# Performance work log

Measured on AMD Instinct MI355X. Metric: run time of the kernel, lower is better.

The kernel has to match this reference:

```python
import jax, jax.numpy as jnp
import numpy as np
from jax import lax

DIM, GC1, GC2, GC3 = 128, 32, 64, 32
B, H, W = 4, 128, 128
EPS = 1e-5


def conv2d(x, w, b, pad, dilation=1, groups=1):
    y = lax.conv_general_dilated(x, w, (1, 1), [(pad, pad), (pad, pad)],
                                 rhs_dilation=(dilation, dilation),
                                 feature_group_count=groups,
                                 dimension_numbers=('NCHW', 'OIHW', 'NCHW'))
    return y + b[None, :, None, None]


def bilinear_gather(img, ys, xs):
    # img [B,C,H,W]; ys,xs [B,K,H,W] float sample coords. Zero padding outside.
    b, c, h, w = img.shape
    k = ys.shape[1]
    flat = img.reshape(b, c, h * w)
    y0 = jnp.floor(ys)
    x0 = jnp.floor(xs)
    acc = jnp.zeros((b, c, k, h, w), img.dtype)
    for dy in (0, 1):
        for dx in (0, 1):
            yc = y0 + dy
            xc = x0 + dx
            wgt = (1.0 - jnp.abs(ys - yc)) * (1.0 - jnp.abs(xs - xc))
            valid = (yc >= 0) & (yc <= h - 1) & (xc >= 0) & (xc <= w - 1)
            yi = jnp.clip(yc, 0, h - 1).astype(jnp.int32)
            xi = jnp.clip(xc, 0, w - 1).astype(jnp.int32)
            idx = (yi * w + xi).reshape(b, 1, k * h * w)
            g = jnp.take_along_axis(flat, jnp.broadcast_to(idx, (b, c, k * h * w)), axis=2)
            g = g.reshape(b, c, k, h, w)
            acc = acc + g * (wgt * valid.astype(img.dtype))[:, None]
    return acc


def deform_depthwise(x, off, w):
    # x [B,C,H,W], off [B,2*9,H,W] (dy,dx interleaved per kernel tap), w [C,9]
    b, c, h, ww = x.shape
    off = off.reshape(b, 9, 2, h, ww)
    dy, dx = off[:, :, 0], off[:, :, 1]  # [B,9,H,W]
    ks = jnp.arange(3, dtype=x.dtype)
    kyy = jnp.repeat(ks, 3)  # [9]
    kxx = jnp.tile(ks, 3)
    iy = jnp.arange(h, dtype=x.dtype)
    jx = jnp.arange(ww, dtype=x.dtype)
    ys = iy[None, None, :, None] - 1.0 + kyy[None, :, None, None] + dy
    xs = jx[None, None, None, :] - 1.0 + kxx[None, :, None, None] + dx
    sampled = bilinear_gather(x, ys, xs)  # [B,C,9,H,W]
    return jnp.einsum('bckhw,ck->bchw', sampled, w)


def batchnorm(x, g, b):
    mu = jnp.mean(x, axis=(0, 2, 3), keepdims=True)
    var = jnp.var(x, axis=(0, 2, 3), keepdims=True)
    return (x - mu) * lax.rsqrt(var + EPS) * g[None, :, None, None] + b[None, :, None, None]


def setup_inputs() -> dict:
    key = jax.random.key(0)
    ks = jax.random.split(key, 16)
    s = 0.05
    return {
        'x': jax.random.normal(ks[0], (B, DIM, H, W), jnp.float32),
        'offset_w': jax.random.normal(ks[1], (18, GC1, 3, 3), jnp.float32) * s,
        'offset_b': jax.random.normal(ks[2], (18,), jnp.float32) * s,
        'deform_w': jax.random.normal(ks[3], (GC1, 9), jnp.float32) * s,
        'dw_w': jax.random.normal(ks[4], (GC2, 1, 7, 7), jnp.float32) * s,
        'dw_b': jax.random.normal(ks[5], (GC2,), jnp.float32) * s,
        'dw2_w': jax.random.normal(ks[6], (GC3, GC3, 3, 3), jnp.float32) * s,
        'dw2_b': jax.random.normal(ks[7], (GC3,), jnp.float32) * s,
        'bn1_g': jnp.ones((DIM,), jnp.float32),
        'bn1_b': jnp.zeros((DIM,), jnp.float32),
        'w1': jax.random.normal(ks[8], (DIM, 4 * DIM), jnp.float32) * s,
        'b1': jax.random.normal(ks[9], (4 * DIM,), jnp.float32) * s,
        'w2': jax.random.normal(ks[10], (4 * DIM, DIM), jnp.float32) * s,
        'b2': jax.random.normal(ks[11], (DIM,), jnp.float32) * s,
        'bn2_g': jnp.ones((DIM,), jnp.float32),
        'bn2_b': jnp.zeros((DIM,), jnp.float32),
    }


def reference(x, offset_w, offset_b, deform_w, dw_w, dw_b, dw2_w, dw2_b,
              bn1_g, bn1_b, w1, b1, w2, b2, bn2_g, bn2_b):
    x_hw, x_w, x_h = jnp.split(x, [GC1, GC1 + GC2], axis=1)
    off = conv2d(x_hw, offset_w, offset_b, pad=1)
    d0 = deform_depthwise(x_hw, off, deform_w)
    d1 = conv2d(x_w, dw_w, dw_b, pad=3, groups=GC2)          # 7x7 depthwise
    d2 = conv2d(x_h, dw2_w, dw2_b, pad=2, dilation=2)        # 3x3 dense, dilation 2
    y = jnp.concatenate([d0, d1, d2], axis=1)
    # channel shuffle, groups=2
    b, c, h, w = y.shape
    y = y.reshape(b, 2, c // 2, h, w).transpose(0, 2, 1, 3, 4).reshape(b, c, h, w)
    y = batchnorm(y, bn1_g, bn1_b)
    t = y.transpose(0, 2, 3, 1)                               # [B,H,W,C]
    t = jax.nn.gelu(t @ w1 + b1, approximate=False)
    t = t @ w2 + b2
    y = t.transpose(0, 3, 1, 2)
    y = batchnorm(y, bn2_g, bn2_b)
    return jax.nn.gelu(x + y, approximate=False)
```

## Files before the change

kernel.cpp:

```cpp
#include <hip/hip_runtime.h>
#include <hip/hip_bf16.h>
#include <math.h>

#define BB 4
#define CC 128
#define HH 128
#define WWD 128
#define HWW 16384
#define PREC 17424

typedef __attribute__((ext_vector_type(8))) short bf16x8;
typedef __attribute__((ext_vector_type(4))) float floatx4;
typedef __attribute__((ext_vector_type(4))) unsigned short us4;
typedef __attribute__((ext_vector_type(8))) unsigned short us8;

__device__ __forceinline__ float gelu_exact(float v) {
  return 0.5f * v * (1.0f + erff(v * 0.70710678118654752f));
}
__device__ __forceinline__ unsigned short f2us(float f) {
  union { float f; unsigned int u; } c; c.f = f;
  unsigned int u = c.u;
  return (unsigned short)((u + 0x7FFFu + ((u >> 16) & 1u)) >> 16);
}

__global__ __launch_bounds__(256) void k_zero(unsigned short* __restrict__ xp) {
  long i = ((long)blockIdx.x * 256 + threadIdx.x) * 8;
  us8 z = (us8)0;
  *(us8*)&xp[i] = z;
}

__global__ __launch_bounds__(256) void k_xt(
    const float* __restrict__ x, float* __restrict__ xt) {
  __shared__ float t[64 * 33];
  int bid = blockIdx.x;
  int tid = threadIdx.x;
  int b = bid >> 8, pg = bid & 255;
  int c = tid >> 3, g8 = tid & 7;
  const float* xp = x + ((long)b * CC + c) * HWW + pg * 64 + g8 * 8;
  float4 v0 = *(const float4*)xp;
  float4 v1 = *(const float4*)(xp + 4);
  t[(g8 * 8 + 0) * 33 + c] = v0.x; t[(g8 * 8 + 1) * 33 + c] = v0.y;
  t[(g8 * 8 + 2) * 33 + c] = v0.z; t[(g8 * 8 + 3) * 33 + c] = v0.w;
  t[(g8 * 8 + 4) * 33 + c] = v1.x; t[(g8 * 8 + 5) * 33 + c] = v1.y;
  t[(g8 * 8 + 6) * 33 + c] = v1.z; t[(g8 * 8 + 7) * 33 + c] = v1.w;
  __syncthreads();
  int u = tid >> 2, q = tid & 3;
  float4 o0, o1;
  o0.x = t[u * 33 + q * 8 + 0]; o0.y = t[u * 33 + q * 8 + 1];
  o0.z = t[u * 33 + q * 8 + 2]; o0.w = t[u * 33 + q * 8 + 3];
  o1.x = t[u * 33 + q * 8 + 4]; o1.y = t[u * 33 + q * 8 + 5];
  o1.z = t[u * 33 + q * 8 + 6]; o1.w = t[u * 33 + q * 8 + 7];
  float* d = xt + ((long)b * HWW + pg * 64 + u) * 32 + q * 8;
  *(float4*)d = o0;
  *(float4*)(d + 4) = o1;
}

__global__ __launch_bounds__(256) void k_pack(
    const float* __restrict__ x, unsigned short* __restrict__ xp) {
  __shared__ float t[64 * 33];
  int bid = blockIdx.x;
  int tid = threadIdx.x;
  int which = bid >> 10, b = (bid >> 8) & 3, pg = bid & 255;
  int cbase = which ? 96 : 0;
  int c = tid >> 3, g8 = tid & 7;
  const float* xpr = x + ((long)b * CC + cbase + c) * HWW + pg * 64 + g8 * 8;
  float4 v0 = *(const float4*)xpr;
  float4 v1 = *(const float4*)(xpr + 4);
  t[(g8 * 8 + 0) * 33 + c] = v0.x; t[(g8 * 8 + 1) * 33 + c] = v0.y;
  t[(g8 * 8 + 2) * 33 + c] = v0.z; t[(g8 * 8 + 3) * 33 + c] = v0.w;
  t[(g8 * 8 + 4) * 33 + c] = v1.x; t[(g8 * 8 + 5) * 33 + c] = v1.y;
  t[(g8 * 8 + 6) * 33 + c] = v1.z; t[(g8 * 8 + 7) * 33 + c] = v1.w;
  __syncthreads();
  int u = tid >> 2, q = tid & 3;
  int p = pg * 64 + u;
  int yy = p >> 7, xx = p & 127;
  long rec = (long)(which * 4 + b) * PREC + (yy + 2) * 132 + xx + 2;
  us8 o;
#pragma unroll
  for (int k = 0; k < 8; k++) o[k] = f2us(t[u * 33 + q * 8 + k]);
  *(us8*)&xp[rec * 32 + q * 8] = o;
}

__global__ __launch_bounds__(256) void k_wprep2(
    const float* __restrict__ offw, const float* __restrict__ dilw,
    unsigned short* __restrict__ wob, unsigned short* __restrict__ w3b) {
  int t = blockIdx.x * 256 + threadIdx.x;
  if (t >= 2304) return;
  int which = t >= 1152;
  int u = t - which * 1152;
  int lane = u & 63, tn = u >> 6;
  int col = lane & 15, quad = lane >> 4;
  int tap = tn >> 1, nt = tn & 1;
  int n = nt * 16 + col;
  const float* W = which ? dilw : offw;
  int noc = which ? 32 : 18;
  unsigned short* d = (which ? w3b : wob) + (long)(tn * 64 + lane) * 8;
#pragma unroll
  for (int j = 0; j < 8; j++)
    d[j] = (n < noc) ? f2us(W[(long)n * 288 + (quad * 8 + j) * 9 + tap]) : (unsigned short)0;
}

__global__ __launch_bounds__(256) void k_offc_mm(
    const unsigned short* __restrict__ xp0, const unsigned short* __restrict__ wob,
    const float* __restrict__ bias, float* __restrict__ off) {
  int bid = blockIdx.x;
  int b = bid >> 7, yy = bid & 127;
  int tid = threadIdx.x;
  int lane = tid & 63, wv = tid >> 6;
  int row = lane & 15, quad = lane >> 4;
  const unsigned short* plane = xp0 + (long)b * PREC * 32;
  int xb = wv * 32;
  floatx4 Oa[2][2];
#pragma unroll
  for (int mt = 0; mt < 2; mt++)
#pragma unroll
    for (int nt = 0; nt < 2; nt++) Oa[mt][nt] = (floatx4)0.f;
#pragma unroll
  for (int t = 0; t < 9; t++) {
    int dy = t / 3 - 1, dx = t % 3 - 1;
    const unsigned short* rp = plane + ((long)(yy + 2 + dy) * 132 + 2 + dx + xb) * 32;
    bf16x8 A0 = *(const bf16x8*)&rp[row * 32 + quad * 8];
    bf16x8 A1 = *(const bf16x8*)&rp[(16 + row) * 32 + quad * 8];
#pragma unroll
    for (int nt = 0; nt < 2; nt++) {
      bf16x8 Bf = *(const bf16x8*)&wob[(long)((t * 2 + nt) * 64 + lane) * 8];
      Oa[0][nt] = __builtin_amdgcn_mfma_f32_16x16x32_bf16(A0, Bf, Oa[0][nt], 0, 0, 0);
      Oa[1][nt] = __builtin_amdgcn_mfma_f32_16x16x32_bf16(A1, Bf, Oa[1][nt], 0, 0, 0);
    }
  }
#pragma unroll
  for (int nt = 0; nt < 2; nt++) {
    int oc = nt * 16 + (lane & 15);
    if (oc < 18) {
      float bb = bias[oc];
#pragma unroll
      for (int mt = 0; mt < 2; mt++) {
        floatx4 v = Oa[mt][nt];
        v[0] += bb; v[1] += bb; v[2] += bb; v[3] += bb;
        long p = (long)(b * 18 + oc) * HWW + yy * 128 + xb + mt * 16 + quad * 4;
        *(floatx4*)&off[p] = v;
      }
    }
  }
}

__global__ __launch_bounds__(256) void k_dil3_mm(
    const unsigned short* __restrict__ xp1, const unsigned short* __restrict__ w3b,
    const float* __restrict__ bias, float* __restrict__ y) {
  int bid = blockIdx.x;
  int b = bid >> 7, yy = bid & 127;
  int tid = threadIdx.x;
  int lane = tid & 63, wv = tid >> 6;
  int row = lane & 15, quad = lane >> 4;
  const unsigned short* plane = xp1 + (long)b * PREC * 32;
  int xb = wv * 32;
  floatx4 Oa[2][2];
#pragma unroll
  for (int mt = 0; mt < 2; mt++)
#pragma unroll
    for (int nt = 0; nt < 2; nt++) Oa[mt][nt] = (floatx4)0.f;
#pragma unroll
  for (int t = 0; t < 9; t++) {
    int dy = (t / 3 - 1) * 2, dx = (t % 3 - 1) * 2;
    const unsigned short* rp = plane + ((long)(yy + 2 + dy) * 132 + 2 + dx + xb) * 32;
    bf16x8 A0 = *(const bf16x8*)&rp[row * 32 + quad * 8];
    bf16x8 A1 = *(const bf16x8*)&rp[(16 + row) * 32 + quad * 8];
#pragma unroll
    for (int nt = 0; nt < 2; nt++) {
      bf16x8 Bf = *(const bf16x8*)&w3b[(long)((t * 2 + nt) * 64 + lane) * 8];
      Oa[0][nt] = __builtin_amdgcn_mfma_f32_16x16x32_bf16(A0, Bf, Oa[0][nt], 0, 0, 0);
      Oa[1][nt] = __builtin_amdgcn_mfma_f32_16x16x32_bf16(A1, Bf, Oa[1][nt], 0, 0, 0);
    }
  }
#pragma unroll
  for (int nt = 0; nt < 2; nt++) {
    int oc = nt * 16 + (lane & 15);
    int cp = 65 + 2 * oc;
    float bb = bias[oc];
#pragma unroll
    for (int mt = 0; mt < 2; mt++) {
      floatx4 v = Oa[mt][nt];
      v[0] += bb; v[1] += bb; v[2] += bb; v[3] += bb;
      long p = ((long)b * CC + cp) * HWW + yy * 128 + xb + mt * 16 + quad * 4;
      *(floatx4*)&y[p] = v;
    }
  }
}

__global__ __launch_bounds__(256) void k_deform(
    const float* __restrict__ xt, const float* __restrict__ off,
    const float* __restrict__ dw, float* __restrict__ y) {
  __shared__ float wl[144];
  int tid = threadIdx.x;
  int g = blockIdx.x * 256 + tid;
  int hf = g >> 16;
  int pix = g & 65535;
  if (tid < 144) {
    int k = tid >> 4, q = tid & 15;
    wl[k * 16 + q] = dw[(hf * 16 + q) * 9 + k];
  }
  __syncthreads();
  int b = pix >> 14, p = pix & 16383;
  int i = p >> 7, j = p & 127;
  float acc[16];
#pragma unroll
  for (int q = 0; q < 16; q++) acc[q] = 0.f;
  const float* offb = off + (long)b * 18 * HWW + p;
  const float* xb = xt + (long)b * HWW * 32 + hf * 16;
  for (int k = 0; k < 9; k++) {
    float dy = offb[(long)(2 * k) * HWW];
    float dx = offb[(long)(2 * k + 1) * HWW];
    float ys = (float)i - 1.f + (float)(k / 3) + dy;
    float xs = (float)j - 1.f + (float)(k % 3) + dx;
    float y0 = floorf(ys), x0 = floorf(xs);
    float fy = ys - y0, fx = xs - x0;
    int iy0 = (int)y0, ix0 = (int)x0;
    int iy1 = iy0 + 1, ix1 = ix0 + 1;
    float wy0 = (1.f - fy) * ((iy0 >= 0 && iy0 <= 127) ? 1.f : 0.f);
    float wy1 = fy * ((iy1 >= 0 && iy1 <= 127) ? 1.f : 0.f);
    float wx0 = (1.f - fx) * ((ix0 >= 0 && ix0 <= 127) ? 1.f : 0.f);
    float wx1 = fx * ((ix1 >= 0 && ix1 <= 127) ? 1.f : 0.f);
    int cy0 = min(max(iy0, 0), 127), cy1 = min(max(iy1, 0), 127);
    int cx0 = min(max(ix0, 0), 127), cx1 = min(max(ix1, 0), 127);
    int ci[4] = {cy0 * 128 + cx0, cy0 * 128 + cx1, cy1 * 128 + cx0, cy1 * 128 + cx1};
    float cw[4] = {wy0 * wx0, wy0 * wx1, wy1 * wx0, wy1 * wx1};
    float v[16];
#pragma unroll
    for (int q = 0; q < 16; q++) v[q] = 0.f;
#pragma unroll
    for (int cn = 0; cn < 4; cn++) {
      const float* cp = xb + (long)ci[cn] * 32;
      float wc = cw[cn];
      float4 p0 = *(const float4*)cp;
      float4 p1 = *(const float4*)(cp + 4);
      float4 p2 = *(const float4*)(cp + 8);
      float4 p3 = *(const float4*)(cp + 12);
      v[0] += wc * p0.x;  v[1] += wc * p0.y;  v[2] += wc * p0.z;  v[3] += wc * p0.w;
      v[4] += wc * p1.x;  v[5] += wc * p1.y;  v[6] += wc * p1.z;  v[7] += wc * p1.w;
      v[8] += wc * p2.x;  v[9] += wc * p2.y;  v[10] += wc * p2.z; v[11] += wc * p2.w;
      v[12] += wc * p3.x; v[13] += wc * p3.y; v[14] += wc * p3.z; v[15] += wc * p3.w;
    }
    const float* wr = &wl[k * 16];
#pragma unroll
    for (int q = 0; q < 16; q++) acc[q] += wr[q] * v[q];
  }
#pragma unroll
  for (int q = 0; q < 16; q++) {
    int cp = 2 * (hf * 16 + q);
    y[((long)b * CC + cp) * HWW + p] = acc[q];
  }
}

__global__ __launch_bounds__(256) void k_dw7(
    const float* __restrict__ x, const float* __restrict__ w,
    const float* __restrict__ bias, float* __restrict__ y) {
  __shared__ float tile[22 * 136];
  __shared__ float wl[49];
  __shared__ float bsh;
  int bid = blockIdx.x;
  int b = bid >> 9, m = (bid >> 3) & 63, strip = bid & 7;
  int r0 = strip * 16;
  int tid = threadIdx.x;
  const float* xp = x + ((long)b * CC + 32 + m) * HWW;
  for (int idx = tid; idx < 2948; idx += 256) {
    int rr = idx / 134;
    int cc = idx - rr * 134 - 3;
    int gy = r0 - 3 + rr;
    float v = 0.f;
    if ((unsigned)gy < 128u && (unsigned)cc < 128u) v = xp[gy * 128 + cc];
    tile[rr * 136 + cc + 3] = v;
  }
  if (tid < 49) wl[tid] = w[m * 49 + tid];
  if (tid == 64) bsh = bias[m];
  __syncthreads();
  int j = tid & 127, s = tid >> 7;
  float acc[8];
#pragma unroll
  for (int o = 0; o < 8; o++) acc[o] = bsh;
#pragma unroll
  for (int kx = 0; kx < 7; kx++) {
#pragma unroll
    for (int rr = 0; rr < 14; rr++) {
      float v = tile[(s * 8 + rr) * 136 + j + kx];
      int olo = rr - 6 > 0 ? rr - 6 : 0;
      int ohi = rr < 7 ? rr : 7;
#pragma unroll
      for (int o = 0; o < 8; o++) {
        if (o >= olo && o <= ohi) acc[o] += v * wl[(rr - o) * 7 + kx];
      }
    }
  }
  int c = 32 + m;
  int cp = (c & 63) * 2 + (c >> 6);
  float* yp = y + ((long)b * CC + cp) * HWW;
#pragma unroll
  for (int o = 0; o < 8; o++) {
    yp[(r0 + s * 8 + o) * 128 + j] = acc[o];
  }
}

__global__ __launch_bounds__(256) void k_stats1(
    const float* __restrict__ buf, float* __restrict__ part) {
  __shared__ float sh[256], sh2[256];
  int c = blockIdx.x >> 2, b = blockIdx.x & 3;
  int tid = threadIdx.x;
  const float* p = buf + ((long)b * CC + c) * HWW;
  float s = 0.f, s2 = 0.f;
  for (int it = 0; it < 16; it++) {
    float4 v = *(const float4*)(p + (it * 256 + tid) * 4);
    s += v.x + v.y + v.z + v.w;
    s2 += v.x * v.x + v.y * v.y + v.z * v.z + v.w * v.w;
  }
  sh[tid] = s; sh2[tid] = s2;
  __syncthreads();
  for (int o = 128; o > 0; o >>= 1) {
    if (tid < o) { sh[tid] += sh[tid + o]; sh2[tid] += sh2[tid + o]; }
    __syncthreads();
  }
  if (tid == 0) {
    part[blockIdx.x * 2] = sh[0];
    part[blockIdx.x * 2 + 1] = sh2[0];
  }
}

__global__ __launch_bounds__(128) void k_stats2(
    const float* __restrict__ part, float* __restrict__ mean, float* __restrict__ istd) {
  int c = threadIdx.x;
  float s = 0.f, s2 = 0.f;
#pragma unroll
  for (int b = 0; b < 4; b++) {
    s += part[(c * 4 + b) * 2];
    s2 += part[(c * 4 + b) * 2 + 1];
  }
  float mu = s * (1.f / 65536.f);
  float var = s2 * (1.f / 65536.f) - mu * mu;
  mean[c] = mu;
  istd[c] = rsqrtf(var + 1e-5f);
}

__global__ __launch_bounds__(256) void k_wprep(
    const float* __restrict__ w1, const float* __restrict__ w2,
    unsigned short* __restrict__ w1b, unsigned short* __restrict__ w2b) {
  int t = blockIdx.x * 256 + threadIdx.x;
  int which = t >> 13;
  int u = t & 8191;
  int lane = u & 63;
  int ntks = u >> 6;
  int col = lane & 15, quad = lane >> 4;
  if (which == 0) {
    int nt = ntks >> 2, ks = ntks & 3;
    int n = nt * 16 + col;
    int k0 = ks * 32 + quad * 8;
    unsigned short* d = w1b + (long)u * 8;
#pragma unroll
    for (int j = 0; j < 8; j++) d[j] = f2us(w1[(long)(k0 + j) * 512 + n]);
  } else {
    int nt = ntks >> 4, ks = ntks & 15;
    int n = nt * 16 + col;
    int k0 = ks * 32 + quad * 8;
    unsigned short* d = w2b + (long)u * 8;
#pragma unroll
    for (int j = 0; j < 8; j++) d[j] = f2us(w2[(long)(k0 + j) * 128 + n]);
  }
}

__global__ __launch_bounds__(256, 2) void k_mlp_mfma(
    const float* __restrict__ y, const float* __restrict__ mean1,
    const float* __restrict__ istd1, const float* __restrict__ g1,
    const float* __restrict__ b1n, const unsigned short* __restrict__ w1b,
    const float* __restrict__ b1, const unsigned short* __restrict__ w2b,
    const float* __restrict__ b2, float* __restrict__ tmid) {
  __shared__ unsigned short At[128 * 136];
  __shared__ unsigned short Hs[4 * 32 * 72];
  __shared__ float scs[128], shs[128];
  int tid = threadIdx.x;
  int lane = tid & 63, wv = tid >> 6;
  int row = lane & 15, quad = lane >> 4;
  int n0 = blockIdx.x * 128;
  int b = n0 >> 14;
  long base = (long)b * CC * HWW + (n0 & 16383);
  if (tid < 128) {
    float sc = istd1[tid] * g1[tid];
    scs[tid] = sc;
    shs[tid] = b1n[tid] - mean1[tid] * sc;
  }
  __syncthreads();
  for (int it = 0; it < 16; it++) {
    int u = it * 256 + tid;
    int tok = u & 127, cg = u >> 7;
    us4 wvv;
#pragma unroll
    for (int r = 0; r < 4; r++) {
      int c = cg * 4 + r;
      float v = y[base + (long)c * HWW + tok];
      wvv[r] = f2us(v * scs[c] + shs[c]);
    }
    *(us4*)&At[tok * 136 + cg * 4] = wvv;
  }
  __syncthreads();
  bf16x8 Af[2][4];
#pragma unroll
  for (int mt = 0; mt < 2; mt++)
#pragma unroll
    for (int ks = 0; ks < 4; ks++)
      Af[mt][ks] = *(const bf16x8*)&At[(wv * 32 + mt * 16 + row) * 136 + ks * 32 + quad * 8];

  floatx4 Oa[2][8];
#pragma unroll
  for (int mt = 0; mt < 2; mt++)
#pragma unroll
    for (int nt = 0; nt < 8; nt++) Oa[mt][nt] = (floatx4)0.f;

  const int wvb = wv * 32 * 72;
  for (int ch = 0; ch < 8; ch++) {
    floatx4 Ha[2][4];
#pragma unroll
    for (int mt = 0; mt < 2; mt++)
#pragma unroll
      for (int nt = 0; nt < 4; nt++) Ha[mt][nt] = (floatx4)0.f;
#pragma unroll
    for (int nt = 0; nt < 4; nt++) {
      int ntg = ch * 4 + nt;
#pragma unroll
      for (int ks = 0; ks < 4; ks++) {
        bf16x8 Bf = *(const bf16x8*)&w1b[(long)(((ntg * 4 + ks) << 6) + lane) * 8];
        Ha[0][nt] = __builtin_amdgcn_mfma_f32_16x16x32_bf16(Af[0][ks], Bf, Ha[0][nt], 0, 0, 0);
        Ha[1][nt] = __builtin_amdgcn_mfma_f32_16x16x32_bf16(Af[1][ks], Bf, Ha[1][nt], 0, 0, 0);
      }
    }
#pragma unroll
    for (int nt = 0; nt < 4; nt++) {
      float bb = b1[ch * 64 + nt * 16 + row];
#pragma unroll
      for (int mt = 0; mt < 2; mt++)
#pragma unroll
        for (int r = 0; r < 4; r++) {
          float h = gelu_exact(Ha[mt][nt][r] + bb);
          Hs[wvb + (mt * 16 + quad * 4 + r) * 72 + nt * 16 + row] = f2us(h);
        }
    }
    __syncthreads();
    bf16x8 A2[2][2];
#pragma unroll
    for (int mt = 0; mt < 2; mt++)
#pragma unroll
      for (int ks = 0; ks < 2; ks++)
        A2[mt][ks] = *(const bf16x8*)&Hs[wvb + (mt * 16 + row) * 72 + ks * 32 + quad * 8];
#pragma unroll
    for (int nt = 0; nt < 8; nt++) {
#pragma unroll
      for (int ks = 0; ks < 2; ks++) {
        bf16x8 Bf = *(const bf16x8*)&w2b[(long)(((nt * 16 + ch * 2 + ks) << 6) + lane) * 8];
        Oa[0][nt] = __builtin_amdgcn_mfma_f32_16x16x32_bf16(A2[0][ks], Bf, Oa[0][nt], 0, 0, 0);
        Oa[1][nt] = __builtin_amdgcn_mfma_f32_16x16x32_bf16(A2[1][ks], Bf, Oa[1][nt], 0, 0, 0);
      }
    }
    __syncthreads();
  }
#pragma unroll
  for (int nt = 0; nt < 8; nt++) {
    int c = nt * 16 + row;
    float bb = b2[c];
    long op = base + (long)c * HWW + wv * 32 + quad * 4;
#pragma unroll
    for (int mt = 0; mt < 2; mt++) {
      floatx4 vv = Oa[mt][nt];
      vv[0] += bb; vv[1] += bb; vv[2] += bb; vv[3] += bb;
      *(floatx4*)&tmid[op + mt * 16] = vv;
    }
  }
}

__global__ __launch_bounds__(256) void k_final(
    const float* __restrict__ x, const float* __restrict__ mean2,
    const float* __restrict__ istd2, const float* __restrict__ g2,
    const float* __restrict__ b2n, float* __restrict__ out) {
  long e4 = (long)blockIdx.x * 256 + threadIdx.x;
  int c = (int)((e4 >> 12) & 127);
  float sc = istd2[c] * g2[c];
  float sh = b2n[c] - mean2[c] * sc;
  float4 o = *(float4*)&out[e4 * 4];
  float4 xv = *(const float4*)&x[e4 * 4];
  o.x = gelu_exact(xv.x + o.x * sc + sh);
  o.y = gelu_exact(xv.y + o.y * sc + sh);
  o.z = gelu_exact(xv.z + o.z * sc + sh);
  o.w = gelu_exact(xv.w + o.w * sc + sh);
  *(float4*)&out[e4 * 4] = o;
}

extern "C" void kernel_launch(void* const* d_in, const int* in_sizes, int n_in,
                              void* d_out, int out_size, void* d_ws, size_t ws_size,
                              hipStream_t stream) {
  const float* x        = (const float*)d_in[0];
  const float* offset_w = (const float*)d_in[1];
  const float* offset_b = (const float*)d_in[2];
  const float* deform_w = (const float*)d_in[3];
  const float* dw_w     = (const float*)d_in[4];
  const float* dw_b     = (const float*)d_in[5];
  const float* dw2_w    = (const float*)d_in[6];
  const float* dw2_b    = (const float*)d_in[7];
  const float* bn1_g    = (const float*)d_in[8];
  const float* bn1_b    = (const float*)d_in[9];
  const float* w1       = (const float*)d_in[10];
  const float* b1       = (const float*)d_in[11];
  const float* w2       = (const float*)d_in[12];
  const float* b2       = (const float*)d_in[13];
  const float* bn2_g    = (const float*)d_in[14];
  const float* bn2_b    = (const float*)d_in[15];
  float* out = (float*)d_out;

  float* ws    = (float*)d_ws;
  float* off   = ws;
  float* ybuf  = ws + 1179648;
  float* stats = ws + 9568256;
  float* mean1 = stats, *istd1 = stats + 128;
  float* mean2 = stats + 256, *istd2 = stats + 384;
  unsigned short* w1b = (unsigned short*)(ws + 9568768);
  unsigned short* w2b = (unsigned short*)(ws + 9601536);
  float* part  = ws + 9634304;
  float* xt    = ws + 9635328;
  unsigned short* wob = (unsigned short*)(ws + 11732480);
  unsigned short* w3b = (unsigned short*)(ws + 11737088);
  unsigned short* xp  = (unsigned short*)(ws + 11741696);
  unsigned short* xp0 = xp;
  unsigned short* xp1 = xp + (long)4 * PREC * 32;
  float* tmid  = out;

  k_zero<<<2178, 256, 0, stream>>>(xp);
  k_wprep<<<64, 256, 0, stream>>>(w1, w2, w1b, w2b);
  k_wprep2<<<9, 256, 0, stream>>>(offset_w, dw2_w, wob, w3b);
  k_pack<<<2048, 256, 0, stream>>>(x, xp);
  k_xt<<<1024, 256, 0, stream>>>(x, xt);
  k_offc_mm<<<512, 256, 0, stream>>>(xp0, wob, offset_b, off);
  k_deform<<<512, 256, 0, stream>>>(xt, off, deform_w, ybuf);
  k_dw7<<<2048, 256, 0, stream>>>(x, dw_w, dw_b, ybuf);
  k_dil3_mm<<<512, 256, 0, stream>>>(xp1, w3b, dw2_b, ybuf);
  k_stats1<<<512, 256, 0, stream>>>(ybuf, part);
  k_stats2<<<1, 128, 0, stream>>>(part, mean1, istd1);
  k_mlp_mfma<<<512, 256, 0, stream>>>(ybuf, mean1, istd1, bn1_g, bn1_b, w1b, b1, w2b, b2, tmid);
  k_stats1<<<512, 256, 0, stream>>>(tmid, part);
  k_stats2<<<1, 128, 0, stream>>>(part, mean2, istd2);
  k_final<<<8192, 256, 0, stream>>>(x, mean2, istd2, bn2_g, bn2_b, out);
}
```

Measured before the change: 278.7 us.

## Fuse BN2 statistics into MLP epilogue and drop inner-loop barriers

The MLP kernel now accumulates per-channel sum and sum-of-squares of its output in shared memory, then adds them atomically to a global buffer. This removes the separate stats pass that re-read the full MLP output, and a zeroing block is added to the existing zero kernel. The first GEMM swaps its operands so each lane holds four consecutive hidden units, which allows vectorized bias loads and us4 stores into the per-wave hidden buffer. Both __syncthreads in the chunk loop are removed because each wave only touches its own Hs slice. The global float atomics make the BN2 statistics order-nondeterministic.

Result: no change. 280.8 us (+0.7%).

```diff
diff --git a/kernel.cpp b/kernel.cpp
--- a/kernel.cpp
+++ b/kernel.cpp
@@ -23,7 +23,9 @@
   return (unsigned short)((u + 0x7FFFu + ((u >> 16) & 1u)) >> 16);
 }
 
-__global__ __launch_bounds__(256) void k_zero(unsigned short* __restrict__ xp) {
+__global__ __launch_bounds__(256) void k_zero(
+    unsigned short* __restrict__ xp, float* __restrict__ part2) {
+  if (blockIdx.x == 2178) { part2[threadIdx.x] = 0.f; return; }
   long i = ((long)blockIdx.x * 256 + threadIdx.x) * 8;
   us8 z = (us8)0;
   *(us8*)&xp[i] = z;
@@ -338,6 +340,15 @@
   istd[c] = rsqrtf(var + 1e-5f);
 }
 
+__global__ __launch_bounds__(128) void k_stats2b(
+    const float* __restrict__ part2, float* __restrict__ mean, float* __restrict__ istd) {
+  int c = threadIdx.x;
+  float mu = part2[c] * (1.f / 65536.f);
+  float var = part2[128 + c] * (1.f / 65536.f) - mu * mu;
+  mean[c] = mu;
+  istd[c] = rsqrtf(var + 1e-5f);
+}
+
 __global__ __launch_bounds__(256) void k_wprep(
     const float* __restrict__ w1, const float* __restrict__ w2,
     unsigned short* __restrict__ w1b, unsigned short* __restrict__ w2b) {
@@ -369,10 +380,12 @@
     const float* __restrict__ istd1, const float* __restrict__ g1,
     const float* __restrict__ b1n, const unsigned short* __restrict__ w1b,
     const float* __restrict__ b1, const unsigned short* __restrict__ w2b,
-    const float* __restrict__ b2, float* __restrict__ tmid) {
+    const float* __restrict__ b2, float* __restrict__ tmid,
+    float* __restrict__ part2) {
   __shared__ unsigned short At[128 * 136];
   __shared__ unsigned short Hs[4 * 32 * 72];
   __shared__ float scs[128], shs[128];
+  __shared__ float ps[128], ps2[128];
   int tid = threadIdx.x;
   int lane = tid & 63, wv = tid >> 6;
   int row = lane & 15, quad = lane >> 4;
@@ -383,6 +396,7 @@
     float sc = istd1[tid] * g1[tid];
     scs[tid] = sc;
     shs[tid] = b1n[tid] - mean1[tid] * sc;
+    ps[tid] = 0.f; ps2[tid] = 0.f;
   }
   __syncthreads();
   for (int it = 0; it < 16; it++) {
@@ -413,33 +427,34 @@
 
   const int wvb = wv * 32 * 72;
   for (int ch = 0; ch < 8; ch++) {
-    floatx4 Ha[2][4];
-#pragma unroll
-    for (int mt = 0; mt < 2; mt++)
-#pragma unroll
-      for (int nt = 0; nt < 4; nt++) Ha[mt][nt] = (floatx4)0.f;
+    floatx4 Ha[4][2];
+#pragma unroll
+    for (int nt = 0; nt < 4; nt++)
+#pragma unroll
+      for (int mt = 0; mt < 2; mt++) Ha[nt][mt] = (floatx4)0.f;
 #pragma unroll
     for (int nt = 0; nt < 4; nt++) {
-      int ntg = ch * 4 + nt;
+      int ht = ch * 4 + nt;
 #pragma unroll
       for (int ks = 0; ks < 4; ks++) {
-        bf16x8 Bf = *(const bf16x8*)&w1b[(long)(((ntg * 4 + ks) << 6) + lane) * 8];
-        Ha[0][nt] = __builtin_amdgcn_mfma_f32_16x16x32_bf16(Af[0][ks], Bf, Ha[0][nt], 0, 0, 0);
-        Ha[1][nt] = __builtin_amdgcn_mfma_f32_16x16x32_bf16(Af[1][ks], Bf, Ha[1][nt], 0, 0, 0);
+        bf16x8 Wf = *(const bf16x8*)&w1b[(long)(((ht * 4 + ks) << 6) + lane) * 8];
+        Ha[nt][0] = __builtin_amdgcn_mfma_f32_16x16x32_bf16(Wf, Af[0][ks], Ha[nt][0], 0, 0, 0);
+        Ha[nt][1] = __builtin_amdgcn_mfma_f32_16x16x32_bf16(Wf, Af[1][ks], Ha[nt][1], 0, 0, 0);
       }
     }
 #pragma unroll
     for (int nt = 0; nt < 4; nt++) {
-      float bb = b1[ch * 64 + nt * 16 + row];
-#pragma unroll
-      for (int mt = 0; mt < 2; mt++)
-#pragma unroll
-        for (int r = 0; r < 4; r++) {
-          float h = gelu_exact(Ha[mt][nt][r] + bb);
-          Hs[wvb + (mt * 16 + quad * 4 + r) * 72 + nt * 16 + row] = f2us(h);
-        }
-    }
-    __syncthreads();
+      float4 bb = *(const float4*)&b1[ch * 64 + nt * 16 + quad * 4];
+#pragma unroll
+      for (int mt = 0; mt < 2; mt++) {
+        us4 hv;
+        hv[0] = f2us(gelu_exact(Ha[nt][mt][0] + bb.x));
+        hv[1] = f2us(gelu_exact(Ha[nt][mt][1] + bb.y));
+        hv[2] = f2us(gelu_exact(Ha[nt][mt][2] + bb.z));
+        hv[3] = f2us(gelu_exact(Ha[nt][mt][3] + bb.w));
+        *(us4*)&Hs[wvb + (mt * 16 + row) * 72 + nt * 16 + quad * 4] = hv;
+      }
+    }
     bf16x8 A2[2][2];
 #pragma unroll
     for (int mt = 0; mt < 2; mt++)
@@ -455,19 +470,28 @@
         Oa[1][nt] = __builtin_amdgcn_mfma_f32_16x16x32_bf16(A2[1][ks], Bf, Oa[1][nt], 0, 0, 0);
       }
     }
-    __syncthreads();
   }
 #pragma unroll
   for (int nt = 0; nt < 8; nt++) {
     int c = nt * 16 + row;
     float bb = b2[c];
     long op = base + (long)c * HWW + wv * 32 + quad * 4;
+    float s = 0.f, s2 = 0.f;
 #pragma unroll
     for (int mt = 0; mt < 2; mt++) {
       floatx4 vv = Oa[mt][nt];
       vv[0] += bb; vv[1] += bb; vv[2] += bb; vv[3] += bb;
       *(floatx4*)&tmid[op + mt * 16] = vv;
-    }
+      s += vv[0] + vv[1] + vv[2] + vv[3];
+      s2 += vv[0] * vv[0] + vv[1] * vv[1] + vv[2] * vv[2] + vv[3] * vv[3];
+    }
+    atomicAdd(&ps[c], s);
+    atomicAdd(&ps2[c], s2);
+  }
+  __syncthreads();
+  if (tid < 128) {
+    atomicAdd(&part2[tid], ps[tid]);
+    atomicAdd(&part2[128 + tid], ps2[tid]);
   }
 }
 
@@ -524,9 +548,10 @@
   unsigned short* xp  = (unsigned short*)(ws + 11741696);
   unsigned short* xp0 = xp;
   unsigned short* xp1 = xp + (long)4 * PREC * 32;
+  float* part2 = ws + 13971968;
   float* tmid  = out;
 
-  k_zero<<<2178, 256, 0, stream>>>(xp);
+  k_zero<<<2179, 256, 0, stream>>>(xp, part2);
   k_wprep<<<64, 256, 0, stream>>>(w1, w2, w1b, w2b);
   k_wprep2<<<9, 256, 0, stream>>>(offset_w, dw2_w, wob, w3b);
   k_pack<<<2048, 256, 0, stream>>>(x, xp);
@@ -537,8 +562,7 @@
   k_dil3_mm<<<512, 256, 0, stream>>>(xp1, w3b, dw2_b, ybuf);
   k_stats1<<<512, 256, 0, stream>>>(ybuf, part);
   k_stats2<<<1, 128, 0, stream>>>(part, mean1, istd1);
-  k_mlp_mfma<<<512, 256, 0, stream>>>(ybuf, mean1, istd1, bn1_g, bn1_b, w1b, b1, w2b, b2, tmid);
-  k_stats1<<<512, 256, 0, stream>>>(tmid, part);
-  k_stats2<<<1, 128, 0, stream>>>(part, mean2, istd2);
+  k_mlp_mfma<<<512, 256, 0, stream>>>(ybuf, mean1, istd1, bn1_g, bn1_b, w1b, b1, w2b, b2, tmid, part2);
+  k_stats2b<<<1, 128, 0, stream>>>(part2, mean2, istd2);
   k_final<<<8192, 256, 0, stream>>>(x, mean2, istd2, bn2_g, bn2_b, out);
 }
```
